# Kernel optimization log

Measured on AMD Instinct MI355X. Metric: run time of the kernel, lower is better.

The kernel has to match this reference:

```python
import jax, jax.numpy as jnp
import numpy as np

S, B, E, H = 2048, 1, 1024, 16
D = E // H                     # head_dim = 64
WINDOW = 1024                  # sliding_window_size
NEG_INF = jnp.float32(-1e30)


def setup_inputs() -> dict:
    key = jax.random.key(0)
    ks = jax.random.split(key, 8)
    w_scale = (2.0 / (E + E)) ** 0.5  # xavier_uniform-ish std
    inp = {
        "query": jax.random.normal(ks[0], (S, B, E), jnp.float32),
        "key": jax.random.normal(ks[1], (S, B, E), jnp.float32),
        "value": jax.random.normal(ks[2], (S, B, E), jnp.float32),
        "positions_bias": jax.random.normal(ks[3], (B * H, S, S), jnp.float32) * 0.1,
        "Wq": jax.random.normal(ks[4], (E, E), jnp.float32) * w_scale,
        "bq": jnp.zeros((E,), jnp.float32),
        "Wk": jax.random.normal(ks[5], (E, E), jnp.float32) * w_scale,
        "bk": jnp.zeros((E,), jnp.float32),
        "Wv": jax.random.normal(ks[6], (E, E), jnp.float32) * w_scale,
        "bv": jnp.zeros((E,), jnp.float32),
        "Wo": jax.random.normal(ks[7], (E, E), jnp.float32) * w_scale,
        "bo": jnp.zeros((E,), jnp.float32),
    }
    return inp


def _heads(x):
    # [S, B, E] -> [B, H, S, D]
    return x.reshape(S, B, H, D).transpose(1, 2, 0, 3)


def _stream(qh, kh, vh, bias, Wo, bo):
    scaling = D ** -0.5
    # NOTE: original pre-scales q by head_dim**-0.5 AND flex_attention applies
    # its default 1/sqrt(head_dim) scale -> effective q.k / head_dim.
    scores = jnp.einsum("bhqd,bhkd->bhqk", qh, kh) * scaling + bias
    qi = jnp.arange(S)[:, None]
    kj = jnp.arange(S)[None, :]
    mask = (qi >= kj) & (qi - kj <= WINDOW)  # causal + sliding window
    scores = jnp.where(mask, scores, NEG_INF)
    p = jax.nn.softmax(scores, axis=-1)
    o = jnp.einsum("bhqk,bhkd->bhqd", p, vh)
    o = o.transpose(2, 0, 1, 3).reshape(S, B, E)  # [S, B, E]
    return o @ Wo.T + bo


def reference(query, key, value, positions_bias, Wq, bq, Wk, bk, Wv, bv, Wo, bo):
    scaling = D ** -0.5
    kh = _heads(key @ Wk.T + bk)
    vh = _heads(value @ Wv.T + bv)
    # query passed as a single tensor -> c == q (non-tuple branch)
    ch = _heads((query @ Wq.T + bq) * scaling)
    bias = positions_bias.reshape(B, H, S, S)
    # content stream (attn_mask=None) and query stream (query_mask=None,
    # query_position_bias defaults to positions_bias) compute identical math
    # here since c == q; XLA will CSE the duplicate.
    c_out = _stream(ch, kh, vh, bias, Wo, bo)
    q_out = _stream(ch, kh, vh, bias, Wo, bo)
    return (c_out, q_out)
```

## Files before the change

kernel.cpp:

```cpp
#include <hip/hip_runtime.h>

typedef unsigned short u16;
typedef __bf16 bf16x8 __attribute__((ext_vector_type(8)));
typedef float f32x4 __attribute__((ext_vector_type(4)));

#define S_LEN 2048
#define EMB   1024
#define NHEAD 16
#define HDIM  64
#define WIN   1024

__device__ __forceinline__ u16 f2bf(float f) {
  unsigned u = __float_as_uint(f);
  u += 0x7FFFu + ((u >> 16) & 1u);
  return (u16)(u >> 16);
}

__global__ __launch_bounds__(256) void conv_kernel(
    const float* __restrict__ p0, const float* __restrict__ p1,
    const float* __restrict__ p2, const float* __restrict__ p3,
    const float* __restrict__ p4, const float* __restrict__ p5,
    const float* __restrict__ p6,
    u16* __restrict__ o0, u16* __restrict__ o1, u16* __restrict__ o2,
    u16* __restrict__ o3, u16* __restrict__ o4, u16* __restrict__ o5,
    u16* __restrict__ o6) {
  const float* src; u16* dst; int n;
  switch (blockIdx.y) {
    case 0: src = p0; dst = o0; n = S_LEN * EMB; break;
    case 1: src = p1; dst = o1; n = S_LEN * EMB; break;
    case 2: src = p2; dst = o2; n = S_LEN * EMB; break;
    case 3: src = p3; dst = o3; n = EMB * EMB; break;
    case 4: src = p4; dst = o4; n = EMB * EMB; break;
    case 5: src = p5; dst = o5; n = EMB * EMB; break;
    default: src = p6; dst = o6; n = EMB * EMB; break;
  }
  int i = (blockIdx.x * 256 + threadIdx.x) * 4;
  if (i >= n) return;
  float4 v = *reinterpret_cast<const float4*>(src + i);
  ushort4 r;
  r.x = f2bf(v.x); r.y = f2bf(v.y); r.z = f2bf(v.z); r.w = f2bf(v.w);
  *reinterpret_cast<ushort4*>(dst + i) = r;
}

__device__ __forceinline__ void gemm_128x64_core(
    const u16* __restrict__ A, const u16* __restrict__ W,
    const float* __restrict__ bias, float scale, int headMajor,
    u16* __restrict__ outB, float* __restrict__ outF0, float* __restrict__ outF1,
    int N, int K, int bm, int bn, u16* As, u16* Bs) {
  const int tid  = threadIdx.x;
  const int w    = tid >> 6;
  const int lane = tid & 63;
  const int wr = w >> 1, wc = w & 1;
  const int lr = lane & 15;
  const int ko = (lane >> 4) * 8;

  f32x4 acc[4][2];
#pragma unroll
  for (int i = 0; i < 4; ++i)
#pragma unroll
    for (int j = 0; j < 2; ++j) acc[i][j] = f32x4{0.f, 0.f, 0.f, 0.f};

  const int srow = lane >> 3;
  const int scol = (lane & 7) * 8;

  for (int k0 = 0; k0 < K; k0 += 64) {
    const u16* Ab = A + (size_t)bm * K + k0;
    const u16* Wb = W + (size_t)bn * K + k0;
#pragma unroll
    for (int c = 0; c < 4; ++c) {
      int s = w * 4 + c;
      __builtin_amdgcn_global_load_lds(
          (const __attribute__((address_space(1))) void*)(Ab + (size_t)(s * 8 + srow) * K + scol),
          (__attribute__((address_space(3))) void*)(As + s * 512), 16, 0, 0);
    }
#pragma unroll
    for (int c = 0; c < 2; ++c) {
      int s = w * 2 + c;
      __builtin_amdgcn_global_load_lds(
          (const __attribute__((address_space(1))) void*)(Wb + (size_t)(s * 8 + srow) * K + scol),
          (__attribute__((address_space(3))) void*)(Bs + s * 512), 16, 0, 0);
    }
    __syncthreads();
#pragma unroll
    for (int kk = 0; kk < 2; ++kk) {
      bf16x8 af[4], bfr[2];
#pragma unroll
      for (int mi = 0; mi < 4; ++mi)
        af[mi] = *reinterpret_cast<const bf16x8*>(&As[(wr * 64 + mi * 16 + lr) * 64 + kk * 32 + ko]);
#pragma unroll
      for (int ni = 0; ni < 2; ++ni)
        bfr[ni] = *reinterpret_cast<const bf16x8*>(&Bs[(wc * 32 + ni * 16 + lr) * 64 + kk * 32 + ko]);
#pragma unroll
      for (int mi = 0; mi < 4; ++mi)
#pragma unroll
        for (int ni = 0; ni < 2; ++ni)
          acc[mi][ni] = __builtin_amdgcn_mfma_f32_16x16x32_bf16(af[mi], bfr[ni], acc[mi][ni], 0, 0, 0);
    }
    __syncthreads();
  }

  const int cr = (lane >> 4) * 4;
  const int cc = lane & 15;
#pragma unroll
  for (int mi = 0; mi < 4; ++mi) {
#pragma unroll
    for (int ni = 0; ni < 2; ++ni) {
      int col = bn + wc * 32 + ni * 16 + cc;
      float bv = bias[col];
#pragma unroll
      for (int r = 0; r < 4; ++r) {
        int row = bm + wr * 64 + mi * 16 + cr + r;
        float val = (acc[mi][ni][r] + bv) * scale;
        if (outB) {
          size_t idx = headMajor
              ? (size_t)(col >> 6) * (S_LEN * HDIM) + (size_t)row * HDIM + (col & 63)
              : (size_t)row * N + col;
          outB[idx] = f2bf(val);
        } else {
          outF0[(size_t)row * N + col] = val;
          outF1[(size_t)row * N + col] = val;
        }
      }
    }
  }
}

__global__ __launch_bounds__(256, 4) void proj_gemm(
    const u16* __restrict__ Abase, const u16* __restrict__ Wbase,
    const float* __restrict__ b0, const float* __restrict__ b1,
    const float* __restrict__ b2, u16* __restrict__ Obase) {
  __shared__ u16 As[128 * 64];
  __shared__ u16 Bs[64 * 64];
  const int z = blockIdx.z;
  const u16* A = Abase + (size_t)z * (S_LEN * EMB);
  const u16* W = Wbase + (size_t)z * (EMB * EMB);
  const float* bias = (z == 0) ? b0 : (z == 1 ? b1 : b2);
  u16* O = Obase + (size_t)z * (S_LEN * EMB);
  float scale = (z == 0) ? (1.0f / 64.0f) : 1.0f;
  gemm_128x64_core(A, W, bias, scale, (z < 2) ? 1 : 0, O, nullptr, nullptr,
                   EMB, EMB, blockIdx.x * 128, blockIdx.y * 64, As, Bs);
}

__global__ __launch_bounds__(256, 4) void out_gemm(
    const u16* __restrict__ A, const u16* __restrict__ W,
    const float* __restrict__ bias, float* __restrict__ out0,
    float* __restrict__ out1) {
  __shared__ u16 As[128 * 64];
  __shared__ u16 Bs[64 * 64];
  gemm_128x64_core(A, W, bias, 1.0f, 0, nullptr, out0, out1,
                   EMB, EMB, blockIdx.x * 128, blockIdx.y * 64, As, Bs);
}

__global__ __launch_bounds__(256) void transpose_v(
    const u16* __restrict__ in, u16* __restrict__ out) {
  __shared__ u16 tile[32][33];
  const int bx = blockIdx.x * 32;
  const int by = blockIdx.y * 32;
  const int tr = threadIdx.x >> 5;
  const int tc = threadIdx.x & 31;
#pragma unroll
  for (int i = 0; i < 4; ++i)
    tile[tr + i * 8][tc] = in[(size_t)(by + tr + i * 8) * EMB + bx + tc];
  __syncthreads();
#pragma unroll
  for (int i = 0; i < 4; ++i)
    out[(size_t)(bx + tr + i * 8) * S_LEN + by + tc] = tile[tc][tr + i * 8];
}

__global__ __launch_bounds__(256, 4) void attn_kernel(
    const u16* __restrict__ Qp, const u16* __restrict__ Kp,
    const u16* __restrict__ Vt, const float* __restrict__ pbias,
    u16* __restrict__ Ob) {
  __shared__ u16 KV[2][2][64 * 64];
  __shared__ u16 Pb[4][16 * 64];

  const int tid  = threadIdx.x;
  const int w    = tid >> 6;
  const int lane = tid & 63;
  const int h  = blockIdx.y;
  const int q0 = (gridDim.x - 1 - blockIdx.x) * 64;
  const int ql = lane & 15;
  const int g  = lane >> 4;
  const int qw = q0 + w * 16;
  const int qg = qw + ql;

  const u16* Kh  = Kp + (size_t)h * (S_LEN * HDIM);
  const u16* Vth = Vt + (size_t)h * (HDIM * S_LEN);

  const u16* Qrow = Qp + (size_t)h * (S_LEN * HDIM) + (size_t)qg * HDIM;
  bf16x8 qf0 = *reinterpret_cast<const bf16x8*>(&Qrow[g * 8]);
  bf16x8 qf1 = *reinterpret_cast<const bf16x8*>(&Qrow[32 + g * 8]);

  f32x4 o[4];
#pragma unroll
  for (int i = 0; i < 4; ++i) o[i] = f32x4{0.f, 0.f, 0.f, 0.f};
  float m = -1e30f, l = 0.f;

  const float* brow = pbias + (size_t)h * S_LEN * S_LEN + (size_t)qg * S_LEN + 4 * g;

  int kv_lo = q0 - WIN; if (kv_lo < 0) kv_lo = 0; kv_lo &= ~63;
  const int ntiles = ((q0 + 63 - kv_lo) >> 6) + 1;
  const int kv_last = kv_lo + (ntiles - 1) * 64;
  const int qw_hi = qw + 15;

  const int swz = (ql & 7) << 4;
  char* Prow = (char*)&Pb[w][0] + ql * 128;

  auto STAGE = [&](int buf, int kv0) {
    u16* Kd = &KV[buf][0][(w * 16) * 64];
    u16* Vd = &KV[buf][1][(w * 16) * 64];
#pragma unroll
    for (int n = 0; n < 2; ++n) {
      int r  = w * 16 + n * 8 + (lane >> 3);
      int cp = (lane & 7) ^ (r & 7);
      __builtin_amdgcn_global_load_lds(
          (const __attribute__((address_space(1))) void*)(Kh + (size_t)(kv0 + r) * HDIM + cp * 8),
          (__attribute__((address_space(3))) void*)(Kd + n * 512), 16, 0, 0);
      __builtin_amdgcn_global_load_lds(
          (const __attribute__((address_space(1))) void*)(Vth + (size_t)r * S_LEN + kv0 + cp * 8),
          (__attribute__((address_space(3))) void*)(Vd + n * 512), 16, 0, 0);
    }
  };

  STAGE(0, kv_lo);
  float4 nb[4], cb[4];
#pragma unroll
  for (int kt = 0; kt < 4; ++kt)
    nb[kt] = *reinterpret_cast<const float4*>(&brow[kv_lo + kt * 16]);
  int cur = 0;

  for (int t = 0; t < ntiles; ++t) {
    const int kv0 = kv_lo + t * 64;
    __syncthreads();
#pragma unroll
    for (int kt = 0; kt < 4; ++kt) cb[kt] = nb[kt];

    if (t + 1 < ntiles) STAGE(cur ^ 1, kv0 + 64);
    const int nxt = (kv0 + 64 <= kv_last) ? kv0 + 64 : kv0;
#pragma unroll
    for (int kt = 0; kt < 4; ++kt)
      nb[kt] = *reinterpret_cast<const float4*>(&brow[nxt + kt * 16]);

    const bool active = (kv0 <= qw_hi) && (kv0 + 63 >= qw - WIN);
    if (active) {
      const char* Kl = (const char*)&KV[cur][0][0];
      const char* Vl = (const char*)&KV[cur][1][0];

      f32x4 s[4];
#pragma unroll
      for (int kt = 0; kt < 4; ++kt) {
        bf16x8 ka = *reinterpret_cast<const bf16x8*>(Kl + (kt * 16 + ql) * 128 + ((g * 16) ^ swz));
        bf16x8 kb = *reinterpret_cast<const bf16x8*>(Kl + (kt * 16 + ql) * 128 + ((64 + g * 16) ^ swz));
        f32x4 acc = f32x4{0.f, 0.f, 0.f, 0.f};
        acc = __builtin_amdgcn_mfma_f32_16x16x32_bf16(ka, qf0, acc, 0, 0, 0);
        acc = __builtin_amdgcn_mfma_f32_16x16x32_bf16(kb, qf1, acc, 0, 0, 0);
        s[kt] = acc;
      }

      const bool full = (kv0 + 63 <= qw) && (qw_hi - kv0 <= WIN);
      float lmax = -INFINITY;
#pragma unroll
      for (int kt = 0; kt < 4; ++kt) {
        float bvr[4] = {cb[kt].x, cb[kt].y, cb[kt].z, cb[kt].w};
#pragma unroll
        for (int r = 0; r < 4; ++r) {
          int k = kv0 + kt * 16 + 4 * g + r;
          float xv = s[kt][r] + bvr[r];
          if (!full) {
            bool ok = (k <= qg) && ((qg - k) <= WIN);
            xv = ok ? xv : -INFINITY;
          }
          s[kt][r] = xv;
          lmax = fmaxf(lmax, xv);
        }
      }
      lmax = fmaxf(lmax, __shfl_xor(lmax, 16));
      lmax = fmaxf(lmax, __shfl_xor(lmax, 32));
      float mn = fmaxf(m, lmax);
      float corr = __expf(m - mn);
      m = mn;
      float ls = 0.f;
#pragma unroll
      for (int kt = 0; kt < 4; ++kt)
#pragma unroll
        for (int r = 0; r < 4; ++r) {
          float e = __expf(s[kt][r] - mn);
          s[kt][r] = e;
          ls += e;
        }
      ls += __shfl_xor(ls, 16);
      ls += __shfl_xor(ls, 32);
      l = l * corr + ls;
#pragma unroll
      for (int dt = 0; dt < 4; ++dt) {
        f32x4 tt = o[dt];
#pragma unroll
        for (int r = 0; r < 4; ++r) tt[r] *= corr;
        o[dt] = tt;
      }

#pragma unroll
      for (int kt = 0; kt < 4; ++kt) {
        ushort4 pw;
        pw.x = f2bf(s[kt][0]); pw.y = f2bf(s[kt][1]);
        pw.z = f2bf(s[kt][2]); pw.w = f2bf(s[kt][3]);
        *reinterpret_cast<ushort4*>(Prow + ((kt * 32 + g * 8) ^ swz)) = pw;
      }
#pragma unroll
      for (int kb = 0; kb < 2; ++kb) {
        bf16x8 pf = *reinterpret_cast<const bf16x8*>(Prow + ((kb * 64 + g * 16) ^ swz));
#pragma unroll
        for (int dt = 0; dt < 4; ++dt) {
          bf16x8 vf = *reinterpret_cast<const bf16x8*>(Vl + (dt * 16 + ql) * 128 + ((kb * 64 + g * 16) ^ swz));
          o[dt] = __builtin_amdgcn_mfma_f32_16x16x32_bf16(vf, pf, o[dt], 0, 0, 0);
        }
      }
    }
    cur ^= 1;
  }

  float inv = (l > 0.f) ? 1.f / l : 0.f;
  u16* op = &Ob[(size_t)qg * EMB + h * HDIM];
#pragma unroll
  for (int dt = 0; dt < 4; ++dt) {
    ushort4 outv;
#pragma unroll
    for (int r = 0; r < 4; ++r) ((u16*)&outv)[r] = f2bf(o[dt][r] * inv);
    *reinterpret_cast<ushort4*>(op + dt * 16 + 4 * g) = outv;
  }
}

extern "C" void kernel_launch(void* const* d_in, const int* in_sizes, int n_in,
                              void* d_out, int out_size, void* d_ws, size_t ws_size,
                              hipStream_t stream) {
  (void)in_sizes; (void)n_in; (void)out_size; (void)ws_size;
  const float* q  = (const float*)d_in[0];
  const float* k  = (const float*)d_in[1];
  const float* v  = (const float*)d_in[2];
  const float* pb = (const float*)d_in[3];
  const float* Wq = (const float*)d_in[4];
  const float* bq = (const float*)d_in[5];
  const float* Wk = (const float*)d_in[6];
  const float* bk = (const float*)d_in[7];
  const float* Wv = (const float*)d_in[8];
  const float* bv = (const float*)d_in[9];
  const float* Wo = (const float*)d_in[10];
  const float* bo = (const float*)d_in[11];
  float* out = (float*)d_out;

  const size_t SE = (size_t)S_LEN * EMB;
  const size_t EE = (size_t)EMB * EMB;
  u16* ws  = (u16*)d_ws;
  u16* qb  = ws;
  u16* kb  = qb + SE;
  u16* vb  = kb + SE;
  u16* wqb = vb + SE;
  u16* wkb = wqb + EE;
  u16* wvb = wkb + EE;
  u16* wob = wvb + EE;
  u16* Qp  = wob + EE;
  u16* Kp  = Qp + SE;
  u16* Vp  = Kp + SE;
  u16* Vt  = Vp + SE;
  u16* Ob  = Vt + SE;

  conv_kernel<<<dim3(2048, 7), 256, 0, stream>>>(q, k, v, Wq, Wk, Wv, Wo,
                                                 qb, kb, vb, wqb, wkb, wvb, wob);
  proj_gemm<<<dim3(16, 16, 3), 256, 0, stream>>>(qb, wqb, bq, bk, bv, Qp);
  transpose_v<<<dim3(32, 64), 256, 0, stream>>>(Vp, Vt);
  attn_kernel<<<dim3(32, 16), 256, 0, stream>>>(Qp, Kp, Vt, pb, Ob);
  out_gemm<<<dim3(16, 16), 256, 0, stream>>>(Ob, wob, bo, out, out + SE);
}
```

Baseline: 103.8 us.

## Fuse V transpose into projection GEMM epilogue and add supertile block ordering

The V projection now writes its output already transposed per head. It stages the tile through LDS with an XOR swizzle and stores it as [head][dim][seq], which removes the separate transpose_v kernel launch and its extra round trip of V through global memory. Both GEMMs also switch to a 1-D grid decoded into 4x4 supertiles, grouping neighbouring blocks so A and W tiles are reused in L2. The cost is an extra LDS pass and barrier in the V epilogue, and the Q/K stores stay scattered as before.

```diff
diff --git a/kernel.cpp b/kernel.cpp
--- a/kernel.cpp
+++ b/kernel.cpp
@@ -9,6 +9,9 @@
 #define NHEAD 16
 #define HDIM  64
 #define WIN   1024
+
+#define AS1 __attribute__((address_space(1)))
+#define AS3 __attribute__((address_space(3)))
 
 __device__ __forceinline__ u16 f2bf(float f) {
   unsigned u = __float_as_uint(f);
@@ -44,7 +47,7 @@
 
 __device__ __forceinline__ void gemm_128x64_core(
     const u16* __restrict__ A, const u16* __restrict__ W,
-    const float* __restrict__ bias, float scale, int headMajor,
+    const float* __restrict__ bias, float scale, int mode,
     u16* __restrict__ outB, float* __restrict__ outF0, float* __restrict__ outF1,
     int N, int K, int bm, int bn, u16* As, u16* Bs) {
   const int tid  = threadIdx.x;
@@ -70,15 +73,15 @@
     for (int c = 0; c < 4; ++c) {
       int s = w * 4 + c;
       __builtin_amdgcn_global_load_lds(
-          (const __attribute__((address_space(1))) void*)(Ab + (size_t)(s * 8 + srow) * K + scol),
-          (__attribute__((address_space(3))) void*)(As + s * 512), 16, 0, 0);
+          (const AS1 void*)(Ab + (size_t)(s * 8 + srow) * K + scol),
+          (AS3 void*)(As + s * 512), 16, 0, 0);
     }
 #pragma unroll
     for (int c = 0; c < 2; ++c) {
       int s = w * 2 + c;
       __builtin_amdgcn_global_load_lds(
-          (const __attribute__((address_space(1))) void*)(Wb + (size_t)(s * 8 + srow) * K + scol),
-          (__attribute__((address_space(3))) void*)(Bs + s * 512), 16, 0, 0);
+          (const AS1 void*)(Wb + (size_t)(s * 8 + srow) * K + scol),
+          (AS3 void*)(Bs + s * 512), 16, 0, 0);
     }
     __syncthreads();
 #pragma unroll
@@ -101,6 +104,37 @@
 
   const int cr = (lane >> 4) * 4;
   const int cc = lane & 15;
+
+  if (mode == 2) {
+#pragma unroll
+    for (int mi = 0; mi < 4; ++mi) {
+#pragma unroll
+      for (int ni = 0; ni < 2; ++ni) {
+        int d = wc * 32 + ni * 16 + cc;
+        float bv = bias[bn + d];
+#pragma unroll
+        for (int r = 0; r < 4; ++r) {
+          int rp = wr * 64 + mi * 16 + cr + r;
+          As[d * 128 + (rp ^ ((d & 7) * 8))] = f2bf((acc[mi][ni][r] + bv) * scale);
+        }
+      }
+    }
+    __syncthreads();
+    const int h = bn >> 6;
+    u16* Vb = outB + (size_t)h * (HDIM * S_LEN);
+    const int dd = tid >> 4;
+    const int ch = tid & 15;
+#pragma unroll
+    for (int i = 0; i < 4; ++i) {
+      int d = dd + i * 16;
+      const u16* src = &As[d * 128 + ((ch ^ (d & 7)) * 8)];
+      u16* dst = Vb + (size_t)d * S_LEN + bm + ch * 8;
+      *reinterpret_cast<ushort4*>(dst)     = *reinterpret_cast<const ushort4*>(src);
+      *reinterpret_cast<ushort4*>(dst + 4) = *reinterpret_cast<const ushort4*>(src + 4);
+    }
+    return;
+  }
+
 #pragma unroll
   for (int mi = 0; mi < 4; ++mi) {
 #pragma unroll
@@ -111,10 +145,8 @@
       for (int r = 0; r < 4; ++r) {
         int row = bm + wr * 64 + mi * 16 + cr + r;
         float val = (acc[mi][ni][r] + bv) * scale;
-        if (outB) {
-          size_t idx = headMajor
-              ? (size_t)(col >> 6) * (S_LEN * HDIM) + (size_t)row * HDIM + (col & 63)
-              : (size_t)row * N + col;
+        if (mode == 1) {
+          size_t idx = (size_t)(col >> 6) * (S_LEN * HDIM) + (size_t)row * HDIM + (col & 63);
           outB[idx] = f2bf(val);
         } else {
           outF0[(size_t)row * N + col] = val;
@@ -125,20 +157,29 @@
   }
 }
 
+__device__ __forceinline__ void supertile_decode(int bx, int& bm, int& bn) {
+  int sb = bx >> 4, inner = bx & 15;
+  bm = ((sb >> 2) * 4 + (inner >> 2)) * 128;
+  bn = ((sb & 3) * 4 + (inner & 3)) * 64;
+}
+
 __global__ __launch_bounds__(256, 4) void proj_gemm(
     const u16* __restrict__ Abase, const u16* __restrict__ Wbase,
     const float* __restrict__ b0, const float* __restrict__ b1,
-    const float* __restrict__ b2, u16* __restrict__ Obase) {
+    const float* __restrict__ b2, u16* __restrict__ Qp,
+    u16* __restrict__ Kp, u16* __restrict__ Vt) {
   __shared__ u16 As[128 * 64];
   __shared__ u16 Bs[64 * 64];
   const int z = blockIdx.z;
   const u16* A = Abase + (size_t)z * (S_LEN * EMB);
   const u16* W = Wbase + (size_t)z * (EMB * EMB);
   const float* bias = (z == 0) ? b0 : (z == 1 ? b1 : b2);
-  u16* O = Obase + (size_t)z * (S_LEN * EMB);
+  u16* O = (z == 0) ? Qp : (z == 1 ? Kp : Vt);
   float scale = (z == 0) ? (1.0f / 64.0f) : 1.0f;
-  gemm_128x64_core(A, W, bias, scale, (z < 2) ? 1 : 0, O, nullptr, nullptr,
-                   EMB, EMB, blockIdx.x * 128, blockIdx.y * 64, As, Bs);
+  int bm, bn;
+  supertile_decode(blockIdx.x, bm, bn);
+  gemm_128x64_core(A, W, bias, scale, (z == 2) ? 2 : 1, O, nullptr, nullptr,
+                   EMB, EMB, bm, bn, As, Bs);
 }
 
 __global__ __launch_bounds__(256, 4) void out_gemm(
@@ -147,24 +188,10 @@
     float* __restrict__ out1) {
   __shared__ u16 As[128 * 64];
   __shared__ u16 Bs[64 * 64];
+  int bm, bn;
+  supertile_decode(blockIdx.x, bm, bn);
   gemm_128x64_core(A, W, bias, 1.0f, 0, nullptr, out0, out1,
-                   EMB, EMB, blockIdx.x * 128, blockIdx.y * 64, As, Bs);
-}
-
-__global__ __launch_bounds__(256) void transpose_v(
-    const u16* __restrict__ in, u16* __restrict__ out) {
-  __shared__ u16 tile[32][33];
-  const int bx = blockIdx.x * 32;
-  const int by = blockIdx.y * 32;
-  const int tr = threadIdx.x >> 5;
-  const int tc = threadIdx.x & 31;
-#pragma unroll
-  for (int i = 0; i < 4; ++i)
-    tile[tr + i * 8][tc] = in[(size_t)(by + tr + i * 8) * EMB + bx + tc];
-  __syncthreads();
-#pragma unroll
-  for (int i = 0; i < 4; ++i)
-    out[(size_t)(bx + tr + i * 8) * S_LEN + by + tc] = tile[tc][tr + i * 8];
+                   EMB, EMB, bm, bn, As, Bs);
 }
 
 __global__ __launch_bounds__(256, 4) void attn_kernel(
@@ -183,6 +210,7 @@
   const int g  = lane >> 4;
   const int qw = q0 + w * 16;
   const int qg = qw + ql;
+  const int qw_hi = qw + 15;
 
   const u16* Kh  = Kp + (size_t)h * (S_LEN * HDIM);
   const u16* Vth = Vt + (size_t)h * (HDIM * S_LEN);
@@ -201,7 +229,6 @@
   int kv_lo = q0 - WIN; if (kv_lo < 0) kv_lo = 0; kv_lo &= ~63;
   const int ntiles = ((q0 + 63 - kv_lo) >> 6) + 1;
   const int kv_last = kv_lo + (ntiles - 1) * 64;
-  const int qw_hi = qw + 15;
 
   const int swz = (ql & 7) << 4;
   char* Prow = (char*)&Pb[w][0] + ql * 128;
@@ -214,11 +241,11 @@
       int r  = w * 16 + n * 8 + (lane >> 3);
       int cp = (lane & 7) ^ (r & 7);
       __builtin_amdgcn_global_load_lds(
-          (const __attribute__((address_space(1))) void*)(Kh + (size_t)(kv0 + r) * HDIM + cp * 8),
-          (__attribute__((address_space(3))) void*)(Kd + n * 512), 16, 0, 0);
+          (const AS1 void*)(Kh + (size_t)(kv0 + r) * HDIM + cp * 8),
+          (AS3 void*)(Kd + n * 512), 16, 0, 0);
       __builtin_amdgcn_global_load_lds(
-          (const __attribute__((address_space(1))) void*)(Vth + (size_t)r * S_LEN + kv0 + cp * 8),
-          (__attribute__((address_space(3))) void*)(Vd + n * 512), 16, 0, 0);
+          (const AS1 void*)(Vth + (size_t)r * S_LEN + kv0 + cp * 8),
+          (AS3 void*)(Vd + n * 512), 16, 0, 0);
     }
   };
 
@@ -360,14 +387,12 @@
   u16* wob = wvb + EE;
   u16* Qp  = wob + EE;
   u16* Kp  = Qp + SE;
-  u16* Vp  = Kp + SE;
-  u16* Vt  = Vp + SE;
+  u16* Vt  = Kp + SE;
   u16* Ob  = Vt + SE;
 
   conv_kernel<<<dim3(2048, 7), 256, 0, stream>>>(q, k, v, Wq, Wk, Wv, Wo,
                                                  qb, kb, vb, wqb, wkb, wvb, wob);
-  proj_gemm<<<dim3(16, 16, 3), 256, 0, stream>>>(qb, wqb, bq, bk, bv, Qp);
-  transpose_v<<<dim3(32, 64), 256, 0, stream>>>(Vp, Vt);
+  proj_gemm<<<dim3(256, 1, 3), 256, 0, stream>>>(qb, wqb, bq, bk, bv, Qp, Kp, Vt);
   attn_kernel<<<dim3(32, 16), 256, 0, stream>>>(Qp, Kp, Vt, pb, Ob);
-  out_gemm<<<dim3(16, 16), 256, 0, stream>>>(Ob, wob, bo, out, out + SE);
-}
+  out_gemm<<<dim3(256), 256, 0, stream>>>(Ob, wob, bo, out, out + SE);
+}
```

Result: faster. 98.54 us (-5.1%).
